# Kernel tuning notes

Hardware: AMD Instinct MI355X
Metric: run time of the kernel (lower is better)

## Reference

```python
import jax, jax.numpy as jnp
import numpy as np

B, C, H, W = 8, 256, 128, 128


def _conv1x1(x, w, b):
    # x: [B,C,H,W], w: [Cout,Cin], b: [Cout]
    return jnp.einsum('oc,bchw->bohw', w, x) + b[None, :, None, None]


def setup_inputs() -> dict:
    key = jax.random.key(0)
    ks = jax.random.split(key, 12)
    s = 1.0 / np.sqrt(C)
    d = {
        'x0': jax.random.normal(ks[0], (B, C, H, W), jnp.float32),
        'x1': jax.random.normal(ks[1], (B, C, H, W), jnp.float32),
        'g_w': jax.random.uniform(ks[2], (C, C), jnp.float32, -s, s),
        'g_b': jax.random.uniform(ks[3], (C,), jnp.float32, -s, s),
        'theta_w': jax.random.uniform(ks[4], (C, C), jnp.float32, -s, s),
        'theta_b': jax.random.uniform(ks[5], (C,), jnp.float32, -s, s),
        'phi_w': jax.random.uniform(ks[6], (C, C), jnp.float32, -s, s),
        'phi_b': jax.random.uniform(ks[7], (C,), jnp.float32, -s, s),
        # Original inits W to zero; use small random weights so output/grads are nontrivial.
        'W_w': jax.random.uniform(ks[8], (C, C), jnp.float32, -s, s) * 0.1,
        'W_b': jax.random.uniform(ks[9], (C,), jnp.float32, -s, s) * 0.1,
    }
    return d


def reference(x0, x1, g_w, g_b, theta_w, theta_b, phi_w, phi_b, W_w, W_b):
    b, c, h, w = x0.shape
    n = h * w
    g_x = _conv1x1(x0, g_w, g_b).reshape(b, c, n)        # [B,C,N]
    theta_x = _conv1x1(x1, theta_w, theta_b).reshape(b, c, n)  # [B,C,N]
    phi_x = _conv1x1(x0, phi_w, phi_b).reshape(b, c, n)   # [B,C,N]
    # f = theta_x @ phi_x^T : [B,C,C]; NO scaling, softmax over dim=1 (columns-normalized)
    f = jnp.einsum('bcn,bdn->bcd', theta_x, phi_x)
    f_div_C = jax.nn.softmax(f, axis=1)
    y = jnp.einsum('bcd,bdn->bcn', f_div_C, g_x)          # [B,C,N]
    # Faithful to torch: permute to [B,N,C] contiguous, then view as [B,C,H,W]
    y = jnp.transpose(y, (0, 2, 1)).reshape(b, c, h, w)
    return _conv1x1(y, W_w, W_b)
```

## Files before the change

### kernel.cpp

```cpp
#include <hip/hip_runtime.h>
#include <hip/hip_bf16.h>
#include <stdint.h>


typedef __attribute__((ext_vector_type(4))) float f32x4;
typedef __attribute__((ext_vector_type(8))) short s16x8;

#define MFMA16(A,B,C) __builtin_amdgcn_mfma_f32_16x16x32_bf16((A),(B),(C),0,0,0)

__device__ __forceinline__ short f2bf(float f) {
    union { float f; uint32_t u; } v; v.f = f;
    uint32_t r = v.u + 0x7fffu + ((v.u >> 16) & 1u);
    return (short)(r >> 16);
}
__device__ __forceinline__ float bf2f(short h) {
    union { uint32_t u; float f; } v; v.u = ((uint32_t)(uint16_t)h) << 16;
    return v.f;
}
__device__ __forceinline__ uint32_t cvtpk(float a, float b) {
    uint32_t r;
    asm("v_cvt_pk_bf16_f32 %0, %1, %2" : "=v"(r) : "v"(a), "v"(b));
    return r;
}
__device__ __forceinline__ void pack2_hl(f32x4 a, f32x4 b, s16x8& hi, s16x8& lo) {
    float v[8] = {a.x,a.y,a.z,a.w,b.x,b.y,b.z,b.w};
    uint32_t h[4]; float r[8];
#pragma unroll
    for (int i=0;i<4;++i) {
        h[i] = cvtpk(v[2*i], v[2*i+1]);
        float f0 = __uint_as_float(h[i] << 16);
        float f1 = __uint_as_float(h[i] & 0xffff0000u);
        r[2*i]   = v[2*i]   - f0;
        r[2*i+1] = v[2*i+1] - f1;
    }
    union { uint32_t u[4]; s16x8 s; } H, L;
#pragma unroll
    for (int i=0;i<4;++i) { H.u[i] = h[i]; L.u[i] = cvtpk(r[2*i], r[2*i+1]); }
    hi = H.s; lo = L.s;
}
__device__ __forceinline__ float hsum4(f32x4 v){ return (v.x+v.y)+(v.z+v.w); }

__global__ __launch_bounds__(256) void k0_prep(
    const float* __restrict__ g_w, const float* __restrict__ W_w,
    short* __restrict__ gwT, short* __restrict__ Wwb,
    float* __restrict__ s0, float* __restrict__ s1)
{
    int gid = blockIdx.x * 256 + threadIdx.x;
    int d = gid >> 8, e = gid & 255;
    gwT[e*256 + d] = f2bf(g_w[gid]);
    Wwb[gid] = f2bf(W_w[gid]);
    if (gid < 2048) { s0[gid] = 0.f; s1[gid] = 0.f; }
}

__global__ __launch_bounds__(256) void k1_gram(
    const float* __restrict__ x0, const float* __restrict__ x1,
    float* __restrict__ partial, float* __restrict__ s0, float* __restrict__ s1)
{
    __shared__ short Ah[128*40], Al[128*40], Bh[128*40], Bl[128*40];
    int bid = blockIdx.x;
    int ij = bid & 3, ch = (bid >> 2) & 31, b = bid >> 7;
    int i0 = (ij >> 1) * 128, j0 = (ij & 1) * 128, k0 = ch * 512;
    int tid = threadIdx.x;
    int w = tid >> 6, lane = tid & 63;
    int wr = (w >> 1) * 64, wc = (w & 1) * 64;
    int quad = lane >> 4, l16 = lane & 15;
    int srow = tid >> 1, skk = (tid & 1) * 16;

    const float* pa = x1 + (size_t)(b*256 + i0 + srow)*16384 + k0 + skk;
    const float* pb = x0 + (size_t)(b*256 + j0 + srow)*16384 + k0 + skk;

    f32x4 acc[4][4];
#pragma unroll
    for (int i=0;i<4;i++)
#pragma unroll
    for (int j=0;j<4;j++) acc[i][j] = f32x4{0.f,0.f,0.f,0.f};

    float sumA = 0.f, sumB = 0.f;

    f32x4 av[4], bv[4];
#pragma unroll
    for (int q=0;q<4;++q) { av[q] = *(const f32x4*)(pa + q*4); bv[q] = *(const f32x4*)(pb + q*4); }
    pa += 32; pb += 32;

    for (int s = 0; s < 16; ++s) {
        __syncthreads();
#pragma unroll
        for (int q=0;q<4;++q) { sumA += hsum4(av[q]); sumB += hsum4(bv[q]); }
        s16x8 h, l;
        pack2_hl(av[0], av[1], h, l);
        ((s16x8*)(Ah + srow*40 + skk))[0] = h; ((s16x8*)(Al + srow*40 + skk))[0] = l;
        pack2_hl(av[2], av[3], h, l);
        ((s16x8*)(Ah + srow*40 + skk))[1] = h; ((s16x8*)(Al + srow*40 + skk))[1] = l;
        pack2_hl(bv[0], bv[1], h, l);
        ((s16x8*)(Bh + srow*40 + skk))[0] = h; ((s16x8*)(Bl + srow*40 + skk))[0] = l;
        pack2_hl(bv[2], bv[3], h, l);
        ((s16x8*)(Bh + srow*40 + skk))[1] = h; ((s16x8*)(Bl + srow*40 + skk))[1] = l;
        __syncthreads();
        f32x4 nav[4], nbv[4];
        if (s < 15) {
#pragma unroll
            for (int q=0;q<4;++q) { nav[q] = *(const f32x4*)(pa + q*4); nbv[q] = *(const f32x4*)(pb + q*4); }
            pa += 32; pb += 32;
        }
        s16x8 ah[4], al[4], bh[4], bl[4];
#pragma unroll
        for (int mt=0; mt<4; ++mt) {
            ah[mt] = *(const s16x8*)(Ah + (wr + mt*16 + l16)*40 + quad*8);
            al[mt] = *(const s16x8*)(Al + (wr + mt*16 + l16)*40 + quad*8);
        }
#pragma unroll
        for (int nt=0; nt<4; ++nt) {
            bh[nt] = *(const s16x8*)(Bh + (wc + nt*16 + l16)*40 + quad*8);
            bl[nt] = *(const s16x8*)(Bl + (wc + nt*16 + l16)*40 + quad*8);
        }
#pragma unroll
        for (int mt=0; mt<4; ++mt)
#pragma unroll
        for (int nt=0; nt<4; ++nt) {
            acc[mt][nt] = MFMA16(ah[mt], bh[nt], acc[mt][nt]);
            acc[mt][nt] = MFMA16(ah[mt], bl[nt], acc[mt][nt]);
            acc[mt][nt] = MFMA16(al[mt], bh[nt], acc[mt][nt]);
        }
        if (s < 15) {
#pragma unroll
            for (int q=0;q<4;++q) { av[q] = nav[q]; bv[q] = nbv[q]; }
        }
    }
    float oA = sumA + __shfl_down(sumA, 1);
    float oB = sumB + __shfl_down(sumB, 1);
    if ((tid & 1) == 0) {
        if (j0 == 0) atomicAdd(&s1[b*256 + i0 + srow], oA);
        if (i0 == 0) atomicAdd(&s0[b*256 + j0 + srow], oB);
    }
    float* outp = partial + (size_t)bid * 16384;
#pragma unroll
    for (int mt=0; mt<4; ++mt)
#pragma unroll
    for (int nt=0; nt<4; ++nt)
#pragma unroll
    for (int r=0; r<4; ++r) {
        int row = wr + mt*16 + quad*4 + r;
        int col = wc + nt*16 + l16;
        outp[row*128 + col] = acc[mt][nt][r];
    }
}

__global__ __launch_bounds__(256) void k1_reduce(
    const float* __restrict__ partial, float* __restrict__ M)
{
    int gid = blockIdx.x*256 + threadIdx.x;
    int b = gid >> 16;
    int rem = gid & 65535;
    int i = rem >> 8, j = rem & 255;
    int ij = ((i>>7)<<1) | (j>>7);
    int idx = (i&127)*128 + (j&127);
    float s = 0.f;
#pragma unroll
    for (int ch = 0; ch < 32; ++ch)
        s += partial[(size_t)((b*32 + ch)*4 + ij)*16384 + idx];
    M[gid] = s;
}

__global__ __launch_bounds__(256) void k2m(
    const float* __restrict__ Tw, const float* __restrict__ Pw,
    const float* __restrict__ pb, const float* __restrict__ s0,
    const float* __restrict__ s1, float* __restrict__ SA, float* __restrict__ SP)
{
    __shared__ float sv[256];
    int b = blockIdx.x >> 1, which = blockIdx.x & 1;
    int t = threadIdx.x;
    sv[t] = which ? s0[b*256 + t] : s1[b*256 + t];
    __syncthreads();
    const float* W = which ? Pw : Tw;
    const float* row = W + t*256;
    float acc = 0.f;
    for (int i = 0; i < 256; ++i) acc += row[i] * sv[i];
    if (which) SP[b*256 + t] = acc + 16384.f * pb[t];
    else       SA[b*256 + t] = acc;
}

__global__ __launch_bounds__(256) void k2a(
    const float* __restrict__ Pw, const float* __restrict__ M, float* __restrict__ P1T)
{
    __shared__ short Ah[128*40], Al[128*40], Bh[128*40], Bl[128*40];
    int bid = blockIdx.x;
    int b = bid >> 2, d0 = ((bid>>1)&1)*128, i0 = (bid&1)*128;
    int tid = threadIdx.x;
    int w = tid >> 6, lane = tid & 63;
    int wr = (w >> 1) * 64, wc = (w & 1) * 64;
    int quad = lane >> 4, l16 = lane & 15;
    int srow = tid >> 1, skk = (tid & 1) * 16;

    f32x4 acc[4][4];
#pragma unroll
    for (int i=0;i<4;i++)
#pragma unroll
    for (int j=0;j<4;j++) acc[i][j] = f32x4{0.f,0.f,0.f,0.f};

    const float* pa0 = Pw + (d0 + srow)*256 + skk;
    const float* pm0 = M + (size_t)b*65536 + (i0 + srow)*256 + skk;

    f32x4 av[4], bv[4];
#pragma unroll
    for (int q=0;q<4;++q) { av[q] = *(const f32x4*)(pa0 + q*4); bv[q] = *(const f32x4*)(pm0 + q*4); }

    for (int s = 0; s < 8; ++s) {
        __syncthreads();
        s16x8 h, l;
        pack2_hl(av[0], av[1], h, l);
        ((s16x8*)(Ah + srow*40 + skk))[0] = h; ((s16x8*)(Al + srow*40 + skk))[0] = l;
        pack2_hl(av[2], av[3], h, l);
        ((s16x8*)(Ah + srow*40 + skk))[1] = h; ((s16x8*)(Al + srow*40 + skk))[1] = l;
        pack2_hl(bv[0], bv[1], h, l);
        ((s16x8*)(Bh + srow*40 + skk))[0] = h; ((s16x8*)(Bl + srow*40 + skk))[0] = l;
        pack2_hl(bv[2], bv[3], h, l);
        ((s16x8*)(Bh + srow*40 + skk))[1] = h; ((s16x8*)(Bl + srow*40 + skk))[1] = l;
        __syncthreads();
        f32x4 nav[4], nbv[4];
        if (s < 7) {
            const float* pa = pa0 + (s+1)*32;
            const float* pm = pm0 + (s+1)*32;
#pragma unroll
            for (int q=0;q<4;++q) { nav[q] = *(const f32x4*)(pa + q*4); nbv[q] = *(const f32x4*)(pm + q*4); }
        }
        s16x8 ah[4], al[4], bh[4], bl[4];
#pragma unroll
        for (int mt=0; mt<4; ++mt) {
            ah[mt] = *(const s16x8*)(Ah + (wr + mt*16 + l16)*40 + quad*8);
            al[mt] = *(const s16x8*)(Al + (wr + mt*16 + l16)*40 + quad*8);
        }
#pragma unroll
        for (int nt=0; nt<4; ++nt) {
            bh[nt] = *(const s16x8*)(Bh + (wc + nt*16 + l16)*40 + quad*8);
            bl[nt] = *(const s16x8*)(Bl + (wc + nt*16 + l16)*40 + quad*8);
        }
#pragma unroll
        for (int mt=0; mt<4; ++mt)
#pragma unroll
        for (int nt=0; nt<4; ++nt) {
            acc[mt][nt] = MFMA16(ah[mt], bh[nt], acc[mt][nt]);
            acc[mt][nt] = MFMA16(ah[mt], bl[nt], acc[mt][nt]);
            acc[mt][nt] = MFMA16(al[mt], bh[nt], acc[mt][nt]);
        }
        if (s < 7) {
#pragma unroll
            for (int q=0;q<4;++q) { av[q] = nav[q]; bv[q] = nbv[q]; }
        }
    }
#pragma unroll
    for (int mt=0; mt<4; ++mt)
#pragma unroll
    for (int nt=0; nt<4; ++nt)
#pragma unroll
    for (int r=0; r<4; ++r) {
        int row = wr + mt*16 + quad*4 + r;
        int col = wc + nt*16 + l16;
        P1T[(size_t)b*65536 + (d0+row)*256 + i0 + col] = acc[mt][nt][r];
    }
}

__global__ __launch_bounds__(256) void k2b1(
    const float* __restrict__ Tw, const float* __restrict__ P1T,
    const float* __restrict__ tb, const float* __restrict__ pb,
    const float* __restrict__ SA, const float* __restrict__ SP,
    float* __restrict__ fws)
{
    __shared__ short Ah[256*40], Al[256*40], Bh[64*40], Bl[64*40];
    int bid = blockIdx.x;
    int b = bid >> 2, d0 = (bid & 3)*64;
    int tid = threadIdx.x;
    int w = tid >> 6, lane = tid & 63;
    int quad = lane >> 4, l16 = lane & 15;

    f32x4 acc[4][4];
#pragma unroll
    for (int i=0;i<4;i++)
#pragma unroll
    for (int j=0;j<4;j++) acc[i][j] = f32x4{0.f,0.f,0.f,0.f};

    const float* pa0 = Tw + tid*256;
    const float* pb0 = P1T + (size_t)b*65536 + (d0 + (tid>>2))*256 + (tid&3)*8;

    f32x4 av[8]; f32x4 bv0, bv1;
#pragma unroll
    for (int q=0;q<8;++q) av[q] = *(const f32x4*)(pa0 + q*4);
    bv0 = *(const f32x4*)(pb0); bv1 = *(const f32x4*)(pb0 + 4);

    for (int s = 0; s < 8; ++s) {
        __syncthreads();
        s16x8 h, l;
#pragma unroll
        for (int q=0;q<4;++q) {
            pack2_hl(av[2*q], av[2*q+1], h, l);
            ((s16x8*)(Ah + tid*40))[q] = h;
            ((s16x8*)(Al + tid*40))[q] = l;
        }
        pack2_hl(bv0, bv1, h, l);
        *(s16x8*)(Bh + (tid>>2)*40 + (tid&3)*8) = h;
        *(s16x8*)(Bl + (tid>>2)*40 + (tid&3)*8) = l;
        __syncthreads();
        f32x4 nav[8], nbv0, nbv1;
        if (s < 7) {
            const float* pa = pa0 + (s+1)*32;
            const float* pbp = pb0 + (s+1)*32;
#pragma unroll
            for (int q=0;q<8;++q) nav[q] = *(const f32x4*)(pa + q*4);
            nbv0 = *(const f32x4*)(pbp); nbv1 = *(const f32x4*)(pbp + 4);
        }
        s16x8 ah[4], al[4], bh[4], bl[4];
#pragma unroll
        for (int mt=0; mt<4; ++mt) {
            ah[mt] = *(const s16x8*)(Ah + (w*64 + mt*16 + l16)*40 + quad*8);
            al[mt] = *(const s16x8*)(Al + (w*64 + mt*16 + l16)*40 + quad*8);
        }
#pragma unroll
        for (int nt=0; nt<4; ++nt) {
            bh[nt] = *(const s16x8*)(Bh + (nt*16 + l16)*40 + quad*8);
            bl[nt] = *(const s16x8*)(Bl + (nt*16 + l16)*40 + quad*8);
        }
#pragma unroll
        for (int mt=0; mt<4; ++mt)
#pragma unroll
        for (int nt=0; nt<4; ++nt) {
            acc[mt][nt] = MFMA16(ah[mt], bh[nt], acc[mt][nt]);
            acc[mt][nt] = MFMA16(ah[mt], bl[nt], acc[mt][nt]);
            acc[mt][nt] = MFMA16(al[mt], bh[nt], acc[mt][nt]);
        }
        if (s < 7) {
#pragma unroll
            for (int q=0;q<8;++q) av[q] = nav[q];
            bv0 = nbv0; bv1 = nbv1;
        }
    }
#pragma unroll
    for (int mt=0; mt<4; ++mt)
#pragma unroll
    for (int nt=0; nt<4; ++nt)
#pragma unroll
    for (int r=0; r<4; ++r) {
        int c = w*64 + mt*16 + quad*4 + r;
        int d = d0 + nt*16 + l16;
        float fv = acc[mt][nt][r] + tb[c]*SP[b*256 + d] + SA[b*256 + c]*pb[d];
        fws[(size_t)b*65536 + d*256 + c] = fv;
    }
}

__global__ __launch_bounds__(256) void k2b2(
    const float* __restrict__ fws, short* __restrict__ F)
{
    int b = blockIdx.x >> 6;
    int d = (blockIdx.x & 63)*4 + (threadIdx.x >> 6);
    int lane = threadIdx.x & 63;
    const float* fr = fws + (size_t)b*65536 + d*256;
    float v[4];
#pragma unroll
    for (int i=0;i<4;++i) v[i] = fr[lane + i*64];
    float mx = fmaxf(fmaxf(v[0],v[1]), fmaxf(v[2],v[3]));
#pragma unroll
    for (int off=32; off>0; off>>=1) mx = fmaxf(mx, __shfl_xor(mx, off));
    float s = 0.f;
#pragma unroll
    for (int i=0;i<4;++i) { v[i] = __expf(v[i] - mx); s += v[i]; }
#pragma unroll
    for (int off=32; off>0; off>>=1) s += __shfl_xor(s, off);
    float inv = 1.f / s;
#pragma unroll
    for (int i=0;i<4;++i)
        F[(size_t)b*65536 + (size_t)(lane + i*64)*256 + d] = f2bf(v[i] * inv);
}

__global__ __launch_bounds__(256) void k2c(
    const short* __restrict__ F, const short* __restrict__ gwT,
    const float* __restrict__ g_b, short* __restrict__ G, float* __restrict__ yb)
{
    int bid = blockIdx.x;
    int b = bid >> 2, c0 = ((bid>>1)&1)*128, e0 = (bid&1)*128;
    int tid = threadIdx.x;
    int w = tid >> 6, lane = tid & 63;
    int wr = (w >> 1) * 64, wc = (w & 1) * 64;
    int quad = lane >> 4, l16 = lane & 15;

    f32x4 acc[4][4];
#pragma unroll
    for (int i=0;i<4;i++)
#pragma unroll
    for (int j=0;j<4;j++) acc[i][j] = f32x4{0.f,0.f,0.f,0.f};

    for (int s = 0; s < 8; ++s) {
        int k0 = s*32;
        s16x8 af[4], bfr[4];
#pragma unroll
        for (int mt=0; mt<4; ++mt)
            af[mt] = *(const s16x8*)(F + (size_t)b*65536 + (c0 + wr + mt*16 + l16)*256 + k0 + quad*8);
#pragma unroll
        for (int nt=0; nt<4; ++nt)
            bfr[nt] = *(const s16x8*)(gwT + (e0 + wc + nt*16 + l16)*256 + k0 + quad*8);
#pragma unroll
        for (int mt=0; mt<4; ++mt)
#pragma unroll
        for (int nt=0; nt<4; ++nt)
            acc[mt][nt] = MFMA16(af[mt], bfr[nt], acc[mt][nt]);
    }
#pragma unroll
    for (int mt=0; mt<4; ++mt)
#pragma unroll
    for (int nt=0; nt<4; ++nt)
#pragma unroll
    for (int r=0; r<4; ++r) {
        int c = c0 + wr + mt*16 + quad*4 + r;
        int e = e0 + wc + nt*16 + l16;
        G[(size_t)b*65536 + c*256 + e] = f2bf(acc[mt][nt][r]);
    }
    if (e0 == 0 && tid < 128) {
        int c = c0 + tid;
        float a = 0.f;
        const short* fr = F + (size_t)b*65536 + c*256;
        for (int d=0; d<256; ++d) a += bf2f(fr[d]) * g_b[d];
        yb[b*256 + c] = a;
    }
}

__global__ __launch_bounds__(256) void k3a(
    const float* __restrict__ x0, const short* __restrict__ G,
    const float* __restrict__ yb, short* __restrict__ yv)
{
    __shared__ short smX[64*40];
    int bid = blockIdx.x;
    int b = bid >> 8, m0 = (bid & 255) * 64;
    int tid = threadIdx.x;
    int w = tid >> 6, lane = tid & 63;
    int quad = lane >> 4, l16 = lane & 15;
    int rc = w * 64;
    int se2 = tid >> 4;
    int g   = tid & 15;
    int keyw = (g >> 1) & 3;

    const float* px = x0 + (size_t)(b*256 + 2*se2)*16384 + m0 + 4*g;
    const short* Gb = G + (size_t)b*65536;
    uint32_t* smDW = (uint32_t*)smX;

    f32x4 acc[4][4];
#pragma unroll
    for (int i=0;i<4;i++)
#pragma unroll
    for (int j=0;j<4;j++) acc[i][j] = f32x4{0.f,0.f,0.f,0.f};

    f32x4 xr0 = *(const f32x4*)(px);
    f32x4 xr1 = *(const f32x4*)(px + 16384);
    px += (size_t)32*16384;
    s16x8 bfr[4];
#pragma unroll
    for (int nt=0; nt<4; ++nt)
        bfr[nt] = *(const s16x8*)(Gb + (rc + nt*16 + l16)*256 + quad*8);

    for (int s = 0; s < 8; ++s) {
        __syncthreads();
        float a0[4] = {xr0.x, xr0.y, xr0.z, xr0.w};
        float a1[4] = {xr1.x, xr1.y, xr1.z, xr1.w};
#pragma unroll
        for (int j=0;j<4;++j) {
            uint32_t u = cvtpk(a0[j], a1[j]);
            smDW[(4*g + j)*20 + (se2 ^ (keyw << 2))] = u;
        }
        __syncthreads();
        f32x4 nx0, nx1; s16x8 nbf[4];
        if (s < 7) {
            nx0 = *(const f32x4*)(px);
            nx1 = *(const f32x4*)(px + 16384);
            px += (size_t)32*16384;
            int e0 = (s+1)*32;
#pragma unroll
            for (int nt=0; nt<4; ++nt)
                nbf[nt] = *(const s16x8*)(Gb + (rc + nt*16 + l16)*256 + e0 + quad*8);
        }
        s16x8 af[4];
#pragma unroll
        for (int mt=0; mt<4; ++mt) {
            int row = mt*16 + l16;
            int kk  = (row >> 3) & 3;
            af[mt] = *(const s16x8*)(smX + row*40 + 8*(quad ^ kk));
        }
#pragma unroll
        for (int mt=0; mt<4; ++mt)
#pragma unroll
        for (int nt=0; nt<4; ++nt)
            acc[mt][nt] = MFMA16(af[mt], bfr[nt], acc[mt][nt]);
        if (s < 7) {
            xr0 = nx0; xr1 = nx1;
#pragma unroll
            for (int nt=0; nt<4; ++nt) bfr[nt] = nbf[nt];
        }
    }
    float ybv[4];
#pragma unroll
    for (int nt=0; nt<4; ++nt) ybv[nt] = yb[b*256 + rc + nt*16 + l16];
    short* base = yv + (size_t)b*4194304 + (size_t)m0*256;
#pragma unroll
    for (int mt=0; mt<4; ++mt)
#pragma unroll
    for (int nt=0; nt<4; ++nt)
#pragma unroll
    for (int r=0; r<4; ++r) {
        int m  = mt*16 + quad*4 + r;
        int rr = rc + nt*16 + l16;
        base[m*256 + rr] = f2bf(acc[mt][nt][r] + ybv[nt]);
    }
}

__global__ __launch_bounds__(256) void k3b(
    const short* __restrict__ yv, const short* __restrict__ Wwb,
    const float* __restrict__ W_b, float* __restrict__ out)
{
    __shared__ short smY[128*40];
    int bid = blockIdx.x;
    int b = bid >> 8, rem = bid & 255;
    int o0 = (rem >> 7) * 128, n0 = (rem & 127) * 128;
    int tid = threadIdx.x;
    int w = tid >> 6, lane = tid & 63;
    int wr = (w >> 1) * 64, wc = (w & 1) * 64;
    int quad = lane >> 4, l16 = lane & 15;
    int p   = tid >> 4;
    int nvg = tid & 15;
    int keyw = nvg & 3;

    const short* py = yv + (size_t)b*4194304 + (size_t)(2*p)*16384 + n0 + nvg*8;
    uint32_t* smDW = (uint32_t*)smY;

    f32x4 acc[4][4];
#pragma unroll
    for (int i=0;i<4;i++)
#pragma unroll
    for (int j=0;j<4;j++) acc[i][j] = f32x4{0.f,0.f,0.f,0.f};

    s16x8 y0 = *(const s16x8*)(py);
    s16x8 y1 = *(const s16x8*)(py + 16384);
    py += (size_t)32*16384;
    s16x8 af[4];
#pragma unroll
    for (int mt=0; mt<4; ++mt)
        af[mt] = *(const s16x8*)(Wwb + (o0 + wr + mt*16 + l16)*256 + quad*8);

    for (int s = 0; s < 8; ++s) {
        __syncthreads();
#pragma unroll
        for (int j=0;j<8;++j) {
            uint32_t u = ((uint32_t)(uint16_t)y0[j]) | ((uint32_t)(uint16_t)y1[j] << 16);
            smDW[(nvg*8 + j)*20 + (p ^ (keyw << 2))] = u;
        }
        __syncthreads();
        s16x8 ny0, ny1, naf[4];
        if (s < 7) {
            ny0 = *(const s16x8*)(py);
            ny1 = *(const s16x8*)(py + 16384);
            py += (size_t)32*16384;
            int c0 = (s+1)*32;
#pragma unroll
            for (int mt=0; mt<4; ++mt)
                naf[mt] = *(const s16x8*)(Wwb + (o0 + wr + mt*16 + l16)*256 + c0 + quad*8);
        }
        s16x8 bfr[4];
#pragma unroll
        for (int nt=0; nt<4; ++nt) {
            int nv = wc + nt*16 + l16;
            int kk = (nv >> 3) & 3;
            bfr[nt] = *(const s16x8*)(smY + nv*40 + 8*(quad ^ kk));
        }
#pragma unroll
        for (int mt=0; mt<4; ++mt)
#pragma unroll
        for (int nt=0; nt<4; ++nt)
            acc[mt][nt] = MFMA16(af[mt], bfr[nt], acc[mt][nt]);
        if (s < 7) {
            y0 = ny0; y1 = ny1;
#pragma unroll
            for (int mt=0; mt<4; ++mt) af[mt] = naf[mt];
        }
    }
#pragma unroll
    for (int mt=0; mt<4; ++mt)
#pragma unroll
    for (int nt=0; nt<4; ++nt)
#pragma unroll
    for (int r=0; r<4; ++r) {
        int o  = o0 + wr + mt*16 + quad*4 + r;
        int nn = n0 + wc + nt*16 + l16;
        out[(size_t)(b*256 + o)*16384 + nn] = acc[mt][nt][r] + W_b[o];
    }
}

extern "C" void kernel_launch(void* const* d_in, const int* in_sizes, int n_in,
                              void* d_out, int out_size, void* d_ws, size_t ws_size,
                              hipStream_t stream)
{
    (void)in_sizes; (void)n_in; (void)out_size; (void)ws_size;
    const float* x0   = (const float*)d_in[0];
    const float* x1   = (const float*)d_in[1];
    const float* g_w  = (const float*)d_in[2];
    const float* g_b  = (const float*)d_in[3];
    const float* th_w = (const float*)d_in[4];
    const float* th_b = (const float*)d_in[5];
    const float* ph_w = (const float*)d_in[6];
    const float* ph_b = (const float*)d_in[7];
    const float* W_w  = (const float*)d_in[8];
    const float* W_b  = (const float*)d_in[9];
    float* out = (float*)d_out;

    char* ws = (char*)d_ws;
    short* yv      = (short*)(ws + 0);
    float* partial = (float*)(ws + 0);
    float* M       = (float*)(ws + 67108864);
    float* P1T     = (float*)(ws + 69206016);
    float* fws     = (float*)(ws + 71303168);
    short* F       = (short*)(ws + 73400320);
    short* G       = (short*)(ws + 74448896);
    short* gwT     = (short*)(ws + 75497472);
    short* Wwb     = (short*)(ws + 75628544);
    float* s0      = (float*)(ws + 75759616);
    float* s1      = (float*)(ws + 75767808);
    float* SA      = (float*)(ws + 75776000);
    float* SP      = (float*)(ws + 75784192);
    float* yb      = (float*)(ws + 75792384);

    k0_prep  <<<dim3(256),  dim3(256), 0, stream>>>(g_w, W_w, gwT, Wwb, s0, s1);
    k1_gram  <<<dim3(1024), dim3(256), 0, stream>>>(x0, x1, partial, s0, s1);
    k1_reduce<<<dim3(2048), dim3(256), 0, stream>>>(partial, M);
    k2m      <<<dim3(16),   dim3(256), 0, stream>>>(th_w, ph_w, ph_b, s0, s1, SA, SP);
    k2a      <<<dim3(32),   dim3(256), 0, stream>>>(ph_w, M, P1T);
    k2b1     <<<dim3(32),   dim3(256), 0, stream>>>(th_w, P1T, th_b, ph_b, SA, SP, fws);
    k2b2     <<<dim3(512),  dim3(256), 0, stream>>>(fws, F);
    k2c      <<<dim3(32),   dim3(256), 0, stream>>>(F, gwT, g_b, G, yb);
    k3a      <<<dim3(2048), dim3(256), 0, stream>>>(x0, G, yb, yv);
    k3b      <<<dim3(2048), dim3(256), 0, stream>>>(yv, Wwb, W_b, out);
}
```

Baseline: 532.8 us.

## Replace split-K partial buffer and reduce kernel with atomic accumulation into M

The gram kernel now atomically adds its 128x128 tile results straight into the final M matrix, which the prep kernel zeroes, instead of writing 32 split-K partials per tile to a 64MB buffer and summing them in a separate reduction kernel. This removes a large write-then-read round trip and one kernel launch. Separately, the register double-buffered global prefetch in the gram loop is dropped, so loads are now issued at the top of each iteration without overlap. The atomics make the summation order nondeterministic and create contention on 32 adds per element, and the lost prefetch may expose load latency.

```diff
diff --git a/kernel.cpp b/kernel.cpp
--- a/kernel.cpp
+++ b/kernel.cpp
@@ -43,18 +43,21 @@
 __global__ __launch_bounds__(256) void k0_prep(
     const float* __restrict__ g_w, const float* __restrict__ W_w,
     short* __restrict__ gwT, short* __restrict__ Wwb,
-    float* __restrict__ s0, float* __restrict__ s1)
+    float* __restrict__ s0, float* __restrict__ s1, float* __restrict__ M)
 {
     int gid = blockIdx.x * 256 + threadIdx.x;
     int d = gid >> 8, e = gid & 255;
     gwT[e*256 + d] = f2bf(g_w[gid]);
     Wwb[gid] = f2bf(W_w[gid]);
     if (gid < 2048) { s0[gid] = 0.f; s1[gid] = 0.f; }
+    f32x4 z = f32x4{0.f,0.f,0.f,0.f};
+    f32x4* mp = (f32x4*)(M + (size_t)gid*8);
+    mp[0] = z; mp[1] = z;
 }
 
 __global__ __launch_bounds__(256) void k1_gram(
     const float* __restrict__ x0, const float* __restrict__ x1,
-    float* __restrict__ partial, float* __restrict__ s0, float* __restrict__ s1)
+    float* __restrict__ M, float* __restrict__ s0, float* __restrict__ s1)
 {
     __shared__ short Ah[128*40], Al[128*40], Bh[128*40], Bl[128*40];
     int bid = blockIdx.x;
@@ -77,15 +80,14 @@
 
     float sumA = 0.f, sumB = 0.f;
 
-    f32x4 av[4], bv[4];
-#pragma unroll
-    for (int q=0;q<4;++q) { av[q] = *(const f32x4*)(pa + q*4); bv[q] = *(const f32x4*)(pb + q*4); }
-    pa += 32; pb += 32;
-
     for (int s = 0; s < 16; ++s) {
-        __syncthreads();
+        f32x4 av[4], bv[4];
+#pragma unroll
+        for (int q=0;q<4;++q) { av[q] = *(const f32x4*)(pa + q*4); bv[q] = *(const f32x4*)(pb + q*4); }
+        pa += 32; pb += 32;
 #pragma unroll
         for (int q=0;q<4;++q) { sumA += hsum4(av[q]); sumB += hsum4(bv[q]); }
+        __syncthreads();
         s16x8 h, l;
         pack2_hl(av[0], av[1], h, l);
         ((s16x8*)(Ah + srow*40 + skk))[0] = h; ((s16x8*)(Al + srow*40 + skk))[0] = l;
@@ -96,12 +98,6 @@
         pack2_hl(bv[2], bv[3], h, l);
         ((s16x8*)(Bh + srow*40 + skk))[1] = h; ((s16x8*)(Bl + srow*40 + skk))[1] = l;
         __syncthreads();
-        f32x4 nav[4], nbv[4];
-        if (s < 15) {
-#pragma unroll
-            for (int q=0;q<4;++q) { nav[q] = *(const f32x4*)(pa + q*4); nbv[q] = *(const f32x4*)(pb + q*4); }
-            pa += 32; pb += 32;
-        }
         s16x8 ah[4], al[4], bh[4], bl[4];
 #pragma unroll
         for (int mt=0; mt<4; ++mt) {
@@ -120,10 +116,6 @@
             acc[mt][nt] = MFMA16(ah[mt], bh[nt], acc[mt][nt]);
             acc[mt][nt] = MFMA16(ah[mt], bl[nt], acc[mt][nt]);
             acc[mt][nt] = MFMA16(al[mt], bh[nt], acc[mt][nt]);
-        }
-        if (s < 15) {
-#pragma unroll
-            for (int q=0;q<4;++q) { av[q] = nav[q]; bv[q] = nbv[q]; }
         }
     }
     float oA = sumA + __shfl_down(sumA, 1);
@@ -132,33 +124,17 @@
         if (j0 == 0) atomicAdd(&s1[b*256 + i0 + srow], oA);
         if (i0 == 0) atomicAdd(&s0[b*256 + j0 + srow], oB);
     }
-    float* outp = partial + (size_t)bid * 16384;
+    float* mb = M + (size_t)b*65536;
 #pragma unroll
     for (int mt=0; mt<4; ++mt)
 #pragma unroll
     for (int nt=0; nt<4; ++nt)
 #pragma unroll
     for (int r=0; r<4; ++r) {
-        int row = wr + mt*16 + quad*4 + r;
-        int col = wc + nt*16 + l16;
-        outp[row*128 + col] = acc[mt][nt][r];
-    }
-}
-
-__global__ __launch_bounds__(256) void k1_reduce(
-    const float* __restrict__ partial, float* __restrict__ M)
-{
-    int gid = blockIdx.x*256 + threadIdx.x;
-    int b = gid >> 16;
-    int rem = gid & 65535;
-    int i = rem >> 8, j = rem & 255;
-    int ij = ((i>>7)<<1) | (j>>7);
-    int idx = (i&127)*128 + (j&127);
-    float s = 0.f;
-#pragma unroll
-    for (int ch = 0; ch < 32; ++ch)
-        s += partial[(size_t)((b*32 + ch)*4 + ij)*16384 + idx];
-    M[gid] = s;
+        int row = i0 + wr + mt*16 + quad*4 + r;
+        int col = j0 + wc + nt*16 + l16;
+        atomicAdd(&mb[row*256 + col], acc[mt][nt][r]);
+    }
 }
 
 __global__ __launch_bounds__(256) void k2m(
@@ -607,7 +583,6 @@
 
     char* ws = (char*)d_ws;
     short* yv      = (short*)(ws + 0);
-    float* partial = (float*)(ws + 0);
     float* M       = (float*)(ws + 67108864);
     float* P1T     = (float*)(ws + 69206016);
     float* fws     = (float*)(ws + 71303168);
@@ -621,9 +596,8 @@
     float* SP      = (float*)(ws + 75784192);
     float* yb      = (float*)(ws + 75792384);
 
-    k0_prep  <<<dim3(256),  dim3(256), 0, stream>>>(g_w, W_w, gwT, Wwb, s0, s1);
-    k1_gram  <<<dim3(1024), dim3(256), 0, stream>>>(x0, x1, partial, s0, s1);
-    k1_reduce<<<dim3(2048), dim3(256), 0, stream>>>(partial, M);
+    k0_prep  <<<dim3(256),  dim3(256), 0, stream>>>(g_w, W_w, gwT, Wwb, s0, s1, M);
+    k1_gram  <<<dim3(1024), dim3(256), 0, stream>>>(x0, x1, M, s0, s1);
     k2m      <<<dim3(16),   dim3(256), 0, stream>>>(th_w, ph_w, ph_b, s0, s1, SA, SP);
     k2a      <<<dim3(32),   dim3(256), 0, stream>>>(ph_w, M, P1T);
     k2b1     <<<dim3(32),   dim3(256), 0, stream>>>(th_w, P1T, th_b, ph_b, SA, SP, fws);
```

Result: no change. 542.1 us (+1.7%).

## Load gram operands directly into MFMA registers, bypassing shared memory

Applied to the files above, without the earlier changes.

The gram kernel no longer stages bf16 hi/lo splits of x0/x1 through LDS. Each lane now loads its MFMA fragment straight from global memory, packs it in registers, and accumulates row sums per wave. This removes the LDS writes, LDS reads and both barriers in each step, but every wave now re-reads rows that other waves also load (2x global/L2 traffic) and uses narrower strided 32-byte accesses. The explicit software prefetch of the next step is gone as well.

```diff
diff --git a/kernel.cpp b/kernel.cpp
--- a/kernel.cpp
+++ b/kernel.cpp
@@ -56,7 +56,6 @@
     const float* __restrict__ x0, const float* __restrict__ x1,
     float* __restrict__ partial, float* __restrict__ s0, float* __restrict__ s1)
 {
-    __shared__ short Ah[128*40], Al[128*40], Bh[128*40], Bl[128*40];
     int bid = blockIdx.x;
     int ij = bid & 3, ch = (bid >> 2) & 31, b = bid >> 7;
     int i0 = (ij >> 1) * 128, j0 = (ij & 1) * 128, k0 = ch * 512;
@@ -64,10 +63,15 @@
     int w = tid >> 6, lane = tid & 63;
     int wr = (w >> 1) * 64, wc = (w & 1) * 64;
     int quad = lane >> 4, l16 = lane & 15;
-    int srow = tid >> 1, skk = (tid & 1) * 16;
-
-    const float* pa = x1 + (size_t)(b*256 + i0 + srow)*16384 + k0 + skk;
-    const float* pb = x0 + (size_t)(b*256 + j0 + srow)*16384 + k0 + skk;
+
+    const float* pa[4];
+    const float* pb[4];
+#pragma unroll
+    for (int mt=0; mt<4; ++mt)
+        pa[mt] = x1 + (size_t)(b*256 + i0 + wr + mt*16 + l16)*16384 + k0 + quad*8;
+#pragma unroll
+    for (int nt=0; nt<4; ++nt)
+        pb[nt] = x0 + (size_t)(b*256 + j0 + wc + nt*16 + l16)*16384 + k0 + quad*8;
 
     f32x4 acc[4][4];
 #pragma unroll
@@ -75,62 +79,62 @@
 #pragma unroll
     for (int j=0;j<4;j++) acc[i][j] = f32x4{0.f,0.f,0.f,0.f};
 
-    float sumA = 0.f, sumB = 0.f;
-
-    f32x4 av[4], bv[4];
-#pragma unroll
-    for (int q=0;q<4;++q) { av[q] = *(const f32x4*)(pa + q*4); bv[q] = *(const f32x4*)(pb + q*4); }
-    pa += 32; pb += 32;
+    float sA[4] = {0.f,0.f,0.f,0.f}, sB[4] = {0.f,0.f,0.f,0.f};
+    const bool doA = (wc == 0) && (j0 == 0);
+    const bool doB = (wr == 0) && (i0 == 0);
 
     for (int s = 0; s < 16; ++s) {
-        __syncthreads();
-#pragma unroll
-        for (int q=0;q<4;++q) { sumA += hsum4(av[q]); sumB += hsum4(bv[q]); }
-        s16x8 h, l;
-        pack2_hl(av[0], av[1], h, l);
-        ((s16x8*)(Ah + srow*40 + skk))[0] = h; ((s16x8*)(Al + srow*40 + skk))[0] = l;
-        pack2_hl(av[2], av[3], h, l);
-        ((s16x8*)(Ah + srow*40 + skk))[1] = h; ((s16x8*)(Al + srow*40 + skk))[1] = l;
-        pack2_hl(bv[0], bv[1], h, l);
-        ((s16x8*)(Bh + srow*40 + skk))[0] = h; ((s16x8*)(Bl + srow*40 + skk))[0] = l;
-        pack2_hl(bv[2], bv[3], h, l);
-        ((s16x8*)(Bh + srow*40 + skk))[1] = h; ((s16x8*)(Bl + srow*40 + skk))[1] = l;
-        __syncthreads();
-        f32x4 nav[4], nbv[4];
-        if (s < 15) {
-#pragma unroll
-            for (int q=0;q<4;++q) { nav[q] = *(const f32x4*)(pa + q*4); nbv[q] = *(const f32x4*)(pb + q*4); }
-            pa += 32; pb += 32;
-        }
-        s16x8 ah[4], al[4], bh[4], bl[4];
+        f32x4 a0[4], a1[4], b0[4], b1[4];
 #pragma unroll
         for (int mt=0; mt<4; ++mt) {
-            ah[mt] = *(const s16x8*)(Ah + (wr + mt*16 + l16)*40 + quad*8);
-            al[mt] = *(const s16x8*)(Al + (wr + mt*16 + l16)*40 + quad*8);
+            a0[mt] = *(const f32x4*)(pa[mt]);
+            a1[mt] = *(const f32x4*)(pa[mt] + 4);
+            pa[mt] += 32;
         }
 #pragma unroll
         for (int nt=0; nt<4; ++nt) {
-            bh[nt] = *(const s16x8*)(Bh + (wc + nt*16 + l16)*40 + quad*8);
-            bl[nt] = *(const s16x8*)(Bl + (wc + nt*16 + l16)*40 + quad*8);
-        }
-#pragma unroll
-        for (int mt=0; mt<4; ++mt)
+            b0[nt] = *(const f32x4*)(pb[nt]);
+            b1[nt] = *(const f32x4*)(pb[nt] + 4);
+            pb[nt] += 32;
+        }
+        if (doA) {
+#pragma unroll
+            for (int mt=0; mt<4; ++mt) sA[mt] += hsum4(a0[mt]) + hsum4(a1[mt]);
+        }
+        if (doB) {
+#pragma unroll
+            for (int nt=0; nt<4; ++nt) sB[nt] += hsum4(b0[nt]) + hsum4(b1[nt]);
+        }
+        s16x8 bh[4], bl[4];
+#pragma unroll
+        for (int nt=0; nt<4; ++nt) pack2_hl(b0[nt], b1[nt], bh[nt], bl[nt]);
+#pragma unroll
+        for (int mt=0; mt<4; ++mt) {
+            s16x8 ah, al;
+            pack2_hl(a0[mt], a1[mt], ah, al);
+#pragma unroll
+            for (int nt=0; nt<4; ++nt) {
+                acc[mt][nt] = MFMA16(ah, bh[nt], acc[mt][nt]);
+                acc[mt][nt] = MFMA16(ah, bl[nt], acc[mt][nt]);
+                acc[mt][nt] = MFMA16(al, bh[nt], acc[mt][nt]);
+            }
+        }
+    }
+    if (doA) {
+#pragma unroll
+        for (int mt=0; mt<4; ++mt) {
+            float v = sA[mt];
+            v += __shfl_xor(v, 16); v += __shfl_xor(v, 32);
+            if (quad == 0) atomicAdd(&s1[b*256 + i0 + wr + mt*16 + l16], v);
+        }
+    }
+    if (doB) {
 #pragma unroll
         for (int nt=0; nt<4; ++nt) {
-            acc[mt][nt] = MFMA16(ah[mt], bh[nt], acc[mt][nt]);
-            acc[mt][nt] = MFMA16(ah[mt], bl[nt], acc[mt][nt]);
-            acc[mt][nt] = MFMA16(al[mt], bh[nt], acc[mt][nt]);
-        }
-        if (s < 15) {
-#pragma unroll
-            for (int q=0;q<4;++q) { av[q] = nav[q]; bv[q] = nbv[q]; }
-        }
-    }
-    float oA = sumA + __shfl_down(sumA, 1);
-    float oB = sumB + __shfl_down(sumB, 1);
-    if ((tid & 1) == 0) {
-        if (j0 == 0) atomicAdd(&s1[b*256 + i0 + srow], oA);
-        if (i0 == 0) atomicAdd(&s0[b*256 + j0 + srow], oB);
+            float v = sB[nt];
+            v += __shfl_xor(v, 16); v += __shfl_xor(v, 32);
+            if (quad == 0) atomicAdd(&s0[b*256 + j0 + wc + nt*16 + l16], v);
+        }
     }
     float* outp = partial + (size_t)bid * 16384;
 #pragma unroll
```

Result: slower. 544.6 us (+2.2%).
